# Optimization experiments

Measured on AMD Instinct MI355X. Metric: run time of the kernel, lower is better.

Reference implementation:

```python
import jax, jax.numpy as jnp
import numpy as np

N, INP, H, FH = 768, 256, 4, 64  # nodes, inp_dim, heads, hidden-per-head (out_dim=H*FH=256)


def setup_inputs() -> dict:
    key = jax.random.key(0)
    k1, k2, k3, k4 = jax.random.split(key, 4)
    x = jax.random.normal(k1, (N, INP), dtype=jnp.float32)
    adj_mat = jax.random.randint(k2, (N, N, 1), 0, 2, dtype=jnp.int32)
    # nn.Linear weights: W.weight [H*FH, INP], a.weight [1, FH] (stored as [FH])
    W = jax.random.uniform(k3, (H * FH, INP), dtype=jnp.float32, minval=-0.1, maxval=0.1)
    a = jax.random.uniform(k4, (FH,), dtype=jnp.float32, minval=-0.1, maxval=0.1)
    return {"x": x, "adj_mat": adj_mat, "W": W, "a": a}


def reference(x, adj_mat, W, a):
    n = x.shape[0]
    Wx = (x @ W.T).reshape(n, H, FH)                       # [N,H,F]
    # dense pairwise features: Wx_ij[i,j] = Wx[i] + Wx[j] (symmetric sum)
    s = Wx[:, None, :, :] + Wx[None, :, :, :]             # [N,N,H,F]
    # dynamic attention: a(leaky_relu(Wx_ij))
    e = jnp.einsum('ijhf,f->ijh', jax.nn.leaky_relu(s, 0.2), a)  # [N,N,H]
    e = jnp.where(adj_mat == 0, -jnp.inf, e)               # adj [N,N,1] broadcasts over H
    att = jax.nn.softmax(e, axis=1)                        # softmax over neighbors j
    # dropout is identity in eval/reference mode
    xh = jnp.einsum('ijh,jhf->ihf', att, Wx)               # [N,H,F]
    return xh.reshape(n, H * FH)                           # concat heads
```

## Files before the change

### kernel.cpp

```cpp
#include <hip/hip_runtime.h>
#include <hip/hip_bf16.h>

#define NN   768
#define INP  256
#define NH   4
#define FH   64
#define DOUT 256

typedef _Float16 h2 __attribute__((ext_vector_type(2)));
typedef _Float16 h8 __attribute__((ext_vector_type(8)));
typedef float    f4 __attribute__((ext_vector_type(4)));

union HU { unsigned int u; h2 h; };
union HS { _Float16 h; unsigned short s; };

__device__ __forceinline__ float b2f(unsigned short u) {
    union { unsigned int i; float f; } v;
    v.i = ((unsigned int)u) << 16;
    return v.f;
}
__device__ __forceinline__ unsigned short f2b(float f) {
    union { float f; unsigned int i; } v; v.f = f;
    unsigned int lsb = (v.i >> 16) & 1;
    v.i += 0x7FFFu + lsb;
    return (unsigned short)(v.i >> 16);
}

__device__ __forceinline__ unsigned int pkadd(unsigned int a, unsigned int b) {
    HU x, y, r; x.u = a; y.u = b; r.h = x.h + y.h; return r.u;
}
#if defined(__has_builtin)
#if __has_builtin(__builtin_amdgcn_fdot2)
#define HAVE_FDOT2 1
#endif
#endif
__device__ __forceinline__ float dot2abs(unsigned int a, unsigned int s, float acc) {
    HU x, y; x.u = a; y.u = s & 0x7FFF7FFFu;
#ifdef HAVE_FDOT2
    return __builtin_amdgcn_fdot2(x.h, y.h, acc, false);
#else
    return acc + (float)x.h.x * (float)y.h.x + (float)x.h.y * (float)y.h.y;
#endif
}

__device__ __forceinline__ int detect_bf16(const void* xin) {
    const unsigned int* xw = (const unsigned int*)xin;
    unsigned int u = xw[(threadIdx.x & 63) * 7];
    unsigned int e = (u >> 7) & 0xFFu;
    unsigned long long m = __ballot(e >= 124u && e <= 127u);
    return (__popcll(m) >= 32) ? 1 : 0;
}

__global__ __launch_bounds__(256) void wx_kernel(
    const void* __restrict__ xin, const void* __restrict__ Win,
    const void* __restrict__ ain,
    _Float16* __restrict__ Wxf, _Float16* __restrict__ BT,
    float* __restrict__ lin, unsigned int* __restrict__ apk,
    int* __restrict__ flagout)
{
    const int isbf = detect_bf16(xin);
    __shared__ float xs[4][INP];
    __shared__ float sa[64];
    const int tid = threadIdx.x;
    const int r0  = blockIdx.x * 4;

    if (isbf) {
        const unsigned short* xp = (const unsigned short*)xin + r0 * INP;
        for (int idx = tid; idx < 4 * INP; idx += 256)
            xs[idx >> 8][idx & 255] = b2f(xp[idx]);
    } else {
        const float* xp = (const float*)xin + r0 * INP;
        for (int idx = tid; idx < 4 * INP; idx += 256)
            xs[idx >> 8][idx & 255] = xp[idx];
    }
    if (tid < 64)
        sa[tid] = isbf ? b2f(((const unsigned short*)ain)[tid])
                       : ((const float*)ain)[tid];
    __syncthreads();

    const int o = tid;
    float acc0 = 0.f, acc1 = 0.f, acc2 = 0.f, acc3 = 0.f;
    if (isbf) {
        const unsigned short* wr = (const unsigned short*)Win + o * INP;
        #pragma unroll 4
        for (int k = 0; k < INP; k += 4) {
            ushort4 u = *(const ushort4*)(wr + k);
            float4 w = make_float4(b2f(u.x), b2f(u.y), b2f(u.z), b2f(u.w));
            float4 x0 = *(const float4*)&xs[0][k];
            float4 x1 = *(const float4*)&xs[1][k];
            float4 x2 = *(const float4*)&xs[2][k];
            float4 x3 = *(const float4*)&xs[3][k];
            acc0 += x0.x * w.x + x0.y * w.y + x0.z * w.z + x0.w * w.w;
            acc1 += x1.x * w.x + x1.y * w.y + x1.z * w.z + x1.w * w.w;
            acc2 += x2.x * w.x + x2.y * w.y + x2.z * w.z + x2.w * w.w;
            acc3 += x3.x * w.x + x3.y * w.y + x3.z * w.z + x3.w * w.w;
        }
    } else {
        const float* wr = (const float*)Win + o * INP;
        #pragma unroll 4
        for (int k = 0; k < INP; k += 4) {
            float4 w = *(const float4*)(wr + k);
            float4 x0 = *(const float4*)&xs[0][k];
            float4 x1 = *(const float4*)&xs[1][k];
            float4 x2 = *(const float4*)&xs[2][k];
            float4 x3 = *(const float4*)&xs[3][k];
            acc0 += x0.x * w.x + x0.y * w.y + x0.z * w.z + x0.w * w.w;
            acc1 += x1.x * w.x + x1.y * w.y + x1.z * w.z + x1.w * w.w;
            acc2 += x2.x * w.x + x2.y * w.y + x2.z * w.z + x2.w * w.w;
            acc3 += x3.x * w.x + x3.y * w.y + x3.z * w.z + x3.w * w.w;
        }
    }

    Wxf[(r0 + 0) * DOUT + o] = (_Float16)acc0;
    Wxf[(r0 + 1) * DOUT + o] = (_Float16)acc1;
    Wxf[(r0 + 2) * DOUT + o] = (_Float16)acc2;
    Wxf[(r0 + 3) * DOUT + o] = (_Float16)acc3;
    {
        HU u0, u1;
        u0.h = h2{(_Float16)acc0, (_Float16)acc1};
        u1.h = h2{(_Float16)acc2, (_Float16)acc3};
        uint2 pv; pv.x = u0.u; pv.y = u1.u;
        *(uint2*)(BT + (size_t)o * NN + r0) = pv;
    }

    const int f = tid & 63;
    const int h = tid >> 6;
    if (blockIdx.x == 0) {
        if (tid == 0) *flagout = isbf;
        if (tid < 32) {
            HU p; p.h = h2{(_Float16)(0.4f * sa[2 * tid]),
                           (_Float16)(0.4f * sa[2 * tid + 1])};
            apk[tid] = p.u;
        }
    }

    const float af = 0.6f * sa[f];
    float v0 = af * acc0, v1 = af * acc1, v2 = af * acc2, v3 = af * acc3;
    #pragma unroll
    for (int d = 1; d < 64; d <<= 1) {
        v0 += __shfl_xor(v0, d);
        v1 += __shfl_xor(v1, d);
        v2 += __shfl_xor(v2, d);
        v3 += __shfl_xor(v3, d);
    }
    if (f == 0) {
        lin[(r0 + 0) * NH + h] = v0;
        lin[(r0 + 1) * NH + h] = v1;
        lin[(r0 + 2) * NH + h] = v2;
        lin[(r0 + 3) * NH + h] = v3;
    }
}

#define ROWP 264
__global__ __launch_bounds__(256, 2) void e_kernel(
    const _Float16* __restrict__ Wxf,
    const float* __restrict__ lin,
    const unsigned int* __restrict__ apk,
    const int* __restrict__ adj,
    _Float16* __restrict__ eH)
{
    __shared__ __align__(16) unsigned short wt[64 * ROWP];

    const int b    = blockIdx.x;
    const int jt   = b % 12, it = b / 12;
    const int i0   = it * 8, j0 = jt * 64;
    const int tid  = threadIdx.x;
    const int h    = tid >> 6;
    const int lane = tid & 63;

    for (int t = tid; t < 64 * 32; t += 256) {
        const int row = t >> 5, c = t & 31;
        const uint4 v = *(const uint4*)(Wxf + (size_t)(j0 + row) * DOUT + c * 8);
        *(uint4*)(&wt[row * ROWP + c * 8]) = v;
    }
    __syncthreads();

    uint4 wj[8], ap[8];
    #pragma unroll
    for (int c = 0; c < 8; ++c)
        wj[c] = *(const uint4*)(&wt[lane * ROWP + h * FH + c * 8]);
    #pragma unroll
    for (int c = 0; c < 8; ++c)
        ap[c] = *(const uint4*)(apk + c * 4);

    const float linj = lin[(j0 + lane) * NH + h];
    const unsigned short NEGINF = 0xFC00;

    #pragma unroll
    for (int ii = 0; ii < 8; ++ii) {
        const int i = i0 + ii;
        const float lini = lin[i * NH + h];
        const int adjv = adj[(size_t)i * NN + j0 + lane];
        float acc = 0.f;
        #pragma unroll
        for (int c = 0; c < 8; ++c) {
            const uint4 wiv = *(const uint4*)(Wxf + (size_t)i * DOUT + h * FH + c * 8);
            acc = dot2abs(ap[c].x, pkadd(wiv.x, wj[c].x), acc);
            acc = dot2abs(ap[c].y, pkadd(wiv.y, wj[c].y), acc);
            acc = dot2abs(ap[c].z, pkadd(wiv.z, wj[c].z), acc);
            acc = dot2abs(ap[c].w, pkadd(wiv.w, wj[c].w), acc);
        }
        const float ev = acc + lini + linj;
        HS hv; hv.h = (_Float16)ev;
        unsigned short st = adjv ? hv.s : NEGINF;
        ((unsigned short*)eH)[((size_t)h * NN + i) * NN + j0 + lane] = st;
    }
}

#define KP 776
__global__ __launch_bounds__(256) void av_kernel(
    const _Float16* __restrict__ eH,
    const _Float16* __restrict__ BT,
    void* __restrict__ outv,
    const int* __restrict__ flag)
{
    __shared__ __align__(16) _Float16 P[16][KP];
    __shared__ float S[16];

    const int b    = blockIdx.x;
    const int h    = b & 3, it = b >> 2;
    const int i0   = it * 16;
    const int tid  = threadIdx.x;
    const int wv   = tid >> 6;
    const int lane = tid & 63;

    #pragma unroll
    for (int rr = 0; rr < 4; ++rr) {
        const int row = wv * 4 + rr;
        const _Float16* er = eH + ((size_t)h * NN + i0 + row) * NN;
        float v[12];
        float m = -__builtin_inff();
        #pragma unroll
        for (int c = 0; c < 12; ++c) {
            v[c] = (float)er[c * 64 + lane];
            m = fmaxf(m, v[c]);
        }
        #pragma unroll
        for (int d = 1; d < 64; d <<= 1) m = fmaxf(m, __shfl_xor(m, d));
        if (m == -__builtin_inff()) m = 0.f;
        float s = 0.f;
        #pragma unroll
        for (int c = 0; c < 12; ++c) {
            const float ev = __expf(v[c] - m);
            s += ev;
            P[row][c * 64 + lane] = (_Float16)ev;
        }
        #pragma unroll
        for (int d = 1; d < 64; d <<= 1) s += __shfl_xor(s, d);
        if (lane == 0) S[row] = fmaxf(s, 1e-30f);
    }
    __syncthreads();

    const int mrow = lane & 15;
    const int quad = lane >> 4;
    const int n0   = wv * 16;
    f4 acc = {0.f, 0.f, 0.f, 0.f};
    const _Float16* bbase = BT + ((size_t)(h * FH + n0 + mrow)) * NN + quad * 8;
    const _Float16* abase = &P[mrow][quad * 8];
    #pragma unroll 4
    for (int k0 = 0; k0 < NN; k0 += 32) {
        const h8 af = *(const h8*)(abase + k0);
        const h8 bf = *(const h8*)(bbase + k0);
        acc = __builtin_amdgcn_mfma_f32_16x16x32_f16(af, bf, acc, 0, 0, 0);
    }

    const int isbf = *flag;
    #pragma unroll
    for (int r = 0; r < 4; ++r) {
        const int row = quad * 4 + r;
        const float val = acc[r] / S[row];
        const size_t oidx = (size_t)(i0 + row) * DOUT + h * FH + n0 + mrow;
        if (isbf) ((unsigned short*)outv)[oidx] = f2b(val);
        else      ((float*)outv)[oidx] = val;
    }
}

extern "C" void kernel_launch(void* const* d_in, const int* in_sizes, int n_in,
                              void* d_out, int out_size, void* d_ws, size_t ws_size,
                              hipStream_t stream) {
    const void* px = d_in[0]; const void* padj = d_in[1];
    const void* pW = d_in[2]; const void* pa  = d_in[3];
    for (int t = 0; t < n_in; ++t) {
        switch (in_sizes[t]) {
            case NN * INP:   px   = d_in[t]; break;
            case NN * NN:    padj = d_in[t]; break;
            case DOUT * INP: pW   = d_in[t]; break;
            case FH:         pa   = d_in[t]; break;
        }
    }

    char* ws = (char*)d_ws;
    int*          flag = (int*)ws;
    unsigned int* apk  = (unsigned int*)(ws + 256);
    float*        lin  = (float*)(ws + 1024);
    _Float16*     Wxf  = (_Float16*)(ws + 16384);
    _Float16*     BT   = (_Float16*)(ws + 409600);
    _Float16*     eH   = (_Float16*)(ws + 802816);

    wx_kernel<<<NN / 4, 256, 0, stream>>>(px, pW, pa, Wxf, BT, lin, apk, flag);
    e_kernel<<<(NN / 8) * (NN / 64), 256, 0, stream>>>(Wxf, lin, apk,
                                                       (const int*)padj, eH);
    av_kernel<<<(NN / 16) * NH, 256, 0, stream>>>(eH, BT, d_out, flag);
}
```

Measured before the change: 98.84 us.

## Fuse attention-score and softmax-aggregation kernels into one per-row-tile kernel

Merges the edge-score kernel and the softmax/MFMA aggregation kernel into a single kernel. Each block now computes the masked scores for 16 rows of one head directly into shared memory as fp32, then runs the softmax and the matrix multiply from there. This removes the fp16 score tensor's round trip through global memory and one kernel launch. In exchange, the score computation runs on only 192 blocks instead of 1152, shared-memory use per block grows, and each lane's neighbour feature rows are read uncoalesced from global memory. Together these may lower occupancy and leave the score phase latency-bound.

```diff
diff --git a/kernel.cpp b/kernel.cpp
--- a/kernel.cpp
+++ b/kernel.cpp
@@ -12,7 +12,6 @@
 typedef float    f4 __attribute__((ext_vector_type(4)));
 
 union HU { unsigned int u; h2 h; };
-union HS { _Float16 h; unsigned short s; };
 
 __device__ __forceinline__ float b2f(unsigned short u) {
     union { unsigned int i; float f; } v;
@@ -151,69 +150,18 @@
     }
 }
 
-#define ROWP 264
-__global__ __launch_bounds__(256, 2) void e_kernel(
+#define EP 772
+#define KP 776
+__global__ __launch_bounds__(256) void gat_kernel(
     const _Float16* __restrict__ Wxf,
+    const _Float16* __restrict__ BT,
     const float* __restrict__ lin,
     const unsigned int* __restrict__ apk,
     const int* __restrict__ adj,
-    _Float16* __restrict__ eH)
-{
-    __shared__ __align__(16) unsigned short wt[64 * ROWP];
-
-    const int b    = blockIdx.x;
-    const int jt   = b % 12, it = b / 12;
-    const int i0   = it * 8, j0 = jt * 64;
-    const int tid  = threadIdx.x;
-    const int h    = tid >> 6;
-    const int lane = tid & 63;
-
-    for (int t = tid; t < 64 * 32; t += 256) {
-        const int row = t >> 5, c = t & 31;
-        const uint4 v = *(const uint4*)(Wxf + (size_t)(j0 + row) * DOUT + c * 8);
-        *(uint4*)(&wt[row * ROWP + c * 8]) = v;
-    }
-    __syncthreads();
-
-    uint4 wj[8], ap[8];
-    #pragma unroll
-    for (int c = 0; c < 8; ++c)
-        wj[c] = *(const uint4*)(&wt[lane * ROWP + h * FH + c * 8]);
-    #pragma unroll
-    for (int c = 0; c < 8; ++c)
-        ap[c] = *(const uint4*)(apk + c * 4);
-
-    const float linj = lin[(j0 + lane) * NH + h];
-    const unsigned short NEGINF = 0xFC00;
-
-    #pragma unroll
-    for (int ii = 0; ii < 8; ++ii) {
-        const int i = i0 + ii;
-        const float lini = lin[i * NH + h];
-        const int adjv = adj[(size_t)i * NN + j0 + lane];
-        float acc = 0.f;
-        #pragma unroll
-        for (int c = 0; c < 8; ++c) {
-            const uint4 wiv = *(const uint4*)(Wxf + (size_t)i * DOUT + h * FH + c * 8);
-            acc = dot2abs(ap[c].x, pkadd(wiv.x, wj[c].x), acc);
-            acc = dot2abs(ap[c].y, pkadd(wiv.y, wj[c].y), acc);
-            acc = dot2abs(ap[c].z, pkadd(wiv.z, wj[c].z), acc);
-            acc = dot2abs(ap[c].w, pkadd(wiv.w, wj[c].w), acc);
-        }
-        const float ev = acc + lini + linj;
-        HS hv; hv.h = (_Float16)ev;
-        unsigned short st = adjv ? hv.s : NEGINF;
-        ((unsigned short*)eH)[((size_t)h * NN + i) * NN + j0 + lane] = st;
-    }
-}
-
-#define KP 776
-__global__ __launch_bounds__(256) void av_kernel(
-    const _Float16* __restrict__ eH,
-    const _Float16* __restrict__ BT,
     void* __restrict__ outv,
     const int* __restrict__ flag)
 {
+    __shared__ float E[16][EP];
     __shared__ __align__(16) _Float16 P[16][KP];
     __shared__ float S[16];
 
@@ -224,30 +172,59 @@
     const int wv   = tid >> 6;
     const int lane = tid & 63;
 
+    uint4 ap[8];
+    #pragma unroll
+    for (int c = 0; c < 8; ++c) ap[c] = *(const uint4*)(apk + c * 4);
+
+    for (int s = 0; s < 3; ++s) {
+        const int j = wv * 192 + s * 64 + lane;
+        uint4 wj[8];
+        #pragma unroll
+        for (int c = 0; c < 8; ++c)
+            wj[c] = *(const uint4*)(Wxf + (size_t)j * DOUT + h * FH + c * 8);
+        const float linj = lin[j * NH + h];
+
+        for (int r = 0; r < 16; ++r) {
+            const int i = i0 + r;
+            const int adjv = adj[(size_t)i * NN + j];
+            const float lini = lin[i * NH + h];
+            float acc = 0.f;
+            #pragma unroll
+            for (int c = 0; c < 8; ++c) {
+                const uint4 wiv = *(const uint4*)(Wxf + (size_t)i * DOUT + h * FH + c * 8);
+                acc = dot2abs(ap[c].x, pkadd(wiv.x, wj[c].x), acc);
+                acc = dot2abs(ap[c].y, pkadd(wiv.y, wj[c].y), acc);
+                acc = dot2abs(ap[c].z, pkadd(wiv.z, wj[c].z), acc);
+                acc = dot2abs(ap[c].w, pkadd(wiv.w, wj[c].w), acc);
+            }
+            E[r][j] = adjv ? (acc + lini + linj) : -__builtin_inff();
+        }
+    }
+    __syncthreads();
+
     #pragma unroll
     for (int rr = 0; rr < 4; ++rr) {
         const int row = wv * 4 + rr;
-        const _Float16* er = eH + ((size_t)h * NN + i0 + row) * NN;
         float v[12];
         float m = -__builtin_inff();
         #pragma unroll
         for (int c = 0; c < 12; ++c) {
-            v[c] = (float)er[c * 64 + lane];
+            v[c] = E[row][c * 64 + lane];
             m = fmaxf(m, v[c]);
         }
         #pragma unroll
         for (int d = 1; d < 64; d <<= 1) m = fmaxf(m, __shfl_xor(m, d));
         if (m == -__builtin_inff()) m = 0.f;
-        float s = 0.f;
+        float sum = 0.f;
         #pragma unroll
         for (int c = 0; c < 12; ++c) {
             const float ev = __expf(v[c] - m);
-            s += ev;
+            sum += ev;
             P[row][c * 64 + lane] = (_Float16)ev;
         }
         #pragma unroll
-        for (int d = 1; d < 64; d <<= 1) s += __shfl_xor(s, d);
-        if (lane == 0) S[row] = fmaxf(s, 1e-30f);
+        for (int d = 1; d < 64; d <<= 1) sum += __shfl_xor(sum, d);
+        if (lane == 0) S[row] = fmaxf(sum, 1e-30f);
     }
     __syncthreads();
 
@@ -295,10 +272,8 @@
     float*        lin  = (float*)(ws + 1024);
     _Float16*     Wxf  = (_Float16*)(ws + 16384);
     _Float16*     BT   = (_Float16*)(ws + 409600);
-    _Float16*     eH   = (_Float16*)(ws + 802816);
 
     wx_kernel<<<NN / 4, 256, 0, stream>>>(px, pW, pa, Wxf, BT, lin, apk, flag);
-    e_kernel<<<(NN / 8) * (NN / 64), 256, 0, stream>>>(Wxf, lin, apk,
-                                                       (const int*)padj, eH);
-    av_kernel<<<(NN / 16) * NH, 256, 0, stream>>>(eH, BT, d_out, flag);
-}
+    gat_kernel<<<(NN / 16) * NH, 256, 0, stream>>>(Wxf, BT, lin, apk,
+                                                   (const int*)padj, d_out, flag);
+}
```

Result: no change. 97.00 us (-1.9%).
